# Kernel tuning notes

Measured on AMD Instinct MI355X. Metric: run time of the kernel, lower is better.

Reference implementation:

```python
import jax, jax.numpy as jnp
import numpy as np
import math

SEQ_LEN = 2048
D_MODEL = 512
HEADS = 8
HEAD_DIM = D_MODEL // HEADS
BATCH = 4


def setup_inputs() -> dict:
    key = jax.random.key(0)
    ks = jax.random.split(key, 12)
    s = 0.02
    return {
        "query": jax.random.normal(ks[0], (BATCH, SEQ_LEN, D_MODEL), dtype=jnp.float32),
        "Wq": jax.random.normal(ks[1], (D_MODEL, D_MODEL), dtype=jnp.float32) * s,
        "bq": jnp.zeros((D_MODEL,), dtype=jnp.float32),
        "Wk": jax.random.normal(ks[2], (D_MODEL, D_MODEL), dtype=jnp.float32) * s,
        "bk": jnp.zeros((D_MODEL,), dtype=jnp.float32),
        "Wv": jax.random.normal(ks[3], (D_MODEL, D_MODEL), dtype=jnp.float32) * s,
        "bv": jnp.zeros((D_MODEL,), dtype=jnp.float32),
        "Wp": jax.random.normal(ks[4], (D_MODEL, D_MODEL), dtype=jnp.float32) * s,
        "bp": jnp.zeros((D_MODEL,), dtype=jnp.float32),
        "logit_scale": jnp.full((HEADS, 1, 1), math.log(10.0), dtype=jnp.float32),
        "rpe": jax.random.normal(ks[5], (2 * SEQ_LEN - 1, HEADS), dtype=jnp.float32) * s,
    }


def reference(query, Wq, bq, Wk, bk, Wv, bv, Wp, bp, logit_scale, rpe):
    N, S, D = query.shape
    H = HEADS

    def split_heads(x):
        # reshape(N, S, head_dim, H) then permute(0, 3, 1, 2) -> (N, H, S, head_dim)
        return x.reshape(N, S, D // H, H).transpose(0, 3, 1, 2)

    q = split_heads(query @ Wq.T + bq)
    k = split_heads(query @ Wk.T + bk)  # key defaults to query
    v = split_heads(query @ Wv.T + bv)  # value defaults to key

    attn = jnp.einsum("bhqd,bhkd->bhqk", q, k) / math.sqrt(D)
    scale = jnp.exp(jnp.minimum(logit_scale, math.log(1.0 / 0.01)))  # (H,1,1)
    attn = attn * scale[None]

    # relative position bias: idx[i,j] = i - j + S - 1
    idx = jnp.arange(S)[:, None] - jnp.arange(S)[None, :] + (S - 1)  # (S,S)
    bias = jax.nn.sigmoid(rpe[idx].transpose(2, 0, 1))  # (H,S,S)
    attn = attn + bias[None]

    attn = jax.nn.softmax(attn, axis=-1)
    out = jnp.einsum("bhqk,bhkd->bhqd", attn, v)
    out = out.transpose(0, 2, 1, 3).reshape(N, S, D)
    return out @ Wp.T + bp
```

## Files before the change

### kernel.cpp

```cpp
#include <hip/hip_runtime.h>
#include <math.h>

#define N_B 4
#define SEQ 2048
#define DM  512
#define H_N 8
#define DH  64

typedef unsigned short ushort_t;
typedef __attribute__((ext_vector_type(8))) short short8_t;
typedef __attribute__((ext_vector_type(4))) float float4_t;

#define LOG2E 1.4426950408889634074f

__device__ __forceinline__ ushort_t f2bf(float f) {
    unsigned int x = __float_as_uint(f);
    unsigned int lsb = (x >> 16) & 1u;
    x += 0x7fffu + lsb;
    return (ushort_t)(x >> 16);
}
__device__ __forceinline__ unsigned int cvtpk_bf16(float a, float b) {
    unsigned int r;
    asm("v_cvt_pk_bf16_f32 %0, %1, %2" : "=v"(r) : "v"(a), "v"(b));
    return r;
}
__device__ __forceinline__ float fexp2(float x) {
#if __has_builtin(__builtin_amdgcn_exp2f)
    return __builtin_amdgcn_exp2f(x);
#else
    return exp2f(x);
#endif
}
__device__ __forceinline__ void gload_lds16(const ushort_t* g, ushort_t* l) {
    __builtin_amdgcn_global_load_lds((const __attribute__((address_space(1))) void*)g,
                                     (__attribute__((address_space(3))) void*)l,
                                     16, 0, 0);
}

#define Q4 1048576
#define W4 65536
#define RELN 4095
#define GTABN (H_N * RELN)
__global__ __launch_bounds__(256)
void prep(const float* __restrict__ query,
          const float* __restrict__ Wq, const float* __restrict__ Wk,
          const float* __restrict__ Wv, const float* __restrict__ Wp,
          const float* __restrict__ bq, const float* __restrict__ bk,
          const float* __restrict__ bv, const float* __restrict__ bp,
          const float* __restrict__ rpe,
          ushort_t* __restrict__ q16, ushort_t* __restrict__ w16,
          float* __restrict__ bcat, float* __restrict__ gtab)
{
    int i = blockIdx.x * 256 + threadIdx.x;
    if (i < Q4) {
        float4 x = ((const float4*)query)[i];
        uint2 p;
        p.x = cvtpk_bf16(x.x, x.y);
        p.y = cvtpk_bf16(x.z, x.w);
        ((uint2*)q16)[i] = p;
    } else if (i < Q4 + 4 * W4) {
        int wi = i - Q4;
        int w = wi >> 16;
        const float* W = (w == 0) ? Wq : (w == 1) ? Wk : (w == 2) ? Wv : Wp;
        float4 x = ((const float4*)W)[wi & (W4 - 1)];
        uint2 p;
        p.x = cvtpk_bf16(x.x, x.y);
        p.y = cvtpk_bf16(x.z, x.w);
        ((uint2*)w16)[wi] = p;
    } else if (i < Q4 + 4 * W4 + 512) {
        int bi = i - (Q4 + 4 * W4);
        int seg = bi >> 7;
        int off = bi & 127;
        const float* B = (seg == 0) ? bq : (seg == 1) ? bk : (seg == 2) ? bv : bp;
        ((float4*)bcat)[bi] = ((const float4*)B)[off];
    } else {
        int gi = i - (Q4 + 4 * W4 + 512);
        if (gi < GTABN) {
            int h = gi / RELN;
            int rel = gi - h * RELN;
            float4 v;
            #pragma unroll
            for (int c = 0; c < 4; c++) {
                int rr = rel - c;
                if (rr < 0) rr = 0;
                float x = rpe[rr * H_N + h];
                ((float*)&v)[c] = LOG2E / (1.0f + __expf(-x));
            }
            ((float4*)gtab)[gi] = v;
        }
    }
}

template<int MODE>
__global__ __launch_bounds__(256)
void mgemm(const ushort_t* __restrict__ A, const ushort_t* __restrict__ B,
           const float* __restrict__ bias,
           ushort_t* __restrict__ q_o, ushort_t* __restrict__ k_o,
           ushort_t* __restrict__ vt_o, float* __restrict__ p_o)
{
    __shared__ __align__(16) ushort_t As[128][64];
    __shared__ __align__(16) ushort_t Bs[128][64];

    const int t     = threadIdx.x;
    const int wid   = t >> 6;
    const int lane  = t & 63;
    const int lan16 = lane & 15;
    const int quad  = lane >> 4;
    const int wm    = (wid & 1) * 64;
    const int wn    = (wid >> 1) * 64;

    const int col0 = blockIdx.x * 128;
    const int row0 = blockIdx.y * 128;

    const int srow = lane >> 3;
    const int gchk = (lane & 7) ^ ((lane >> 3) & 7);
    const ushort_t* gA = A + (size_t)(row0 + wid * 8 + srow) * DM + gchk * 8;
    const ushort_t* gB = B + (size_t)(col0 + wid * 8 + srow) * DM + gchk * 8;

    float4_t acc[4][4];
    #pragma unroll
    for (int i = 0; i < 4; i++)
        #pragma unroll
        for (int j = 0; j < 4; j++) acc[i][j] = (float4_t){0.f, 0.f, 0.f, 0.f};

    const int sw = lan16 & 7;

    for (int k0 = 0; k0 < DM; k0 += 64) {
        __syncthreads();
        #pragma unroll
        for (int j = 0; j < 4; j++) {
            gload_lds16(gA + k0 + (size_t)j * 32 * DM, &As[j * 32 + wid * 8][0]);
            gload_lds16(gB + k0 + (size_t)j * 32 * DM, &Bs[j * 32 + wid * 8][0]);
        }
        asm volatile("s_waitcnt vmcnt(0)" ::: "memory");
        __syncthreads();

        #pragma unroll
        for (int kk = 0; kk < 2; kk++) {
            short8_t af[4], bf[4];
            #pragma unroll
            for (int i = 0; i < 4; i++) {
                af[i] = *(const short8_t*)&As[wm + i * 16 + lan16][((kk * 4 + quad) ^ sw) * 8];
                bf[i] = *(const short8_t*)&Bs[wn + i * 16 + lan16][((kk * 4 + quad) ^ sw) * 8];
            }
            #pragma unroll
            for (int i = 0; i < 4; i++)
                #pragma unroll
                for (int j = 0; j < 4; j++)
                    acc[i][j] = __builtin_amdgcn_mfma_f32_16x16x32_bf16(af[i], bf[j], acc[i][j], 0, 0, 0);
        }
    }

    #pragma unroll
    for (int j = 0; j < 4; j++) {
        int col = col0 + wn + j * 16 + lan16;
        float bv = bias[col];
        #pragma unroll
        for (int i = 0; i < 4; i++) {
            #pragma unroll
            for (int reg = 0; reg < 4; reg++) {
                int row = row0 + wm + i * 16 + quad * 4 + reg;
                float v = acc[i][j][reg] + bv;
                if (MODE == 0) {
                    int w = col >> 9;
                    int c = col & 511;
                    int hh = c & 7, dh = c >> 3;
                    int n = row >> 11, s = row & 2047;
                    if (w == 0)
                        q_o[(((size_t)(n * H_N + hh)) * SEQ + s) * DH + dh] = f2bf(v);
                    else if (w == 1)
                        k_o[(((size_t)(n * H_N + hh)) * SEQ + s) * DH + dh] = f2bf(v);
                    else
                        vt_o[(((size_t)(n * H_N + hh)) * DH + dh) * SEQ + s] = f2bf(v);
                } else {
                    p_o[(size_t)row * DM + col] = v;
                }
            }
        }
    }
}

__global__ __launch_bounds__(256)
void attn_k(const ushort_t* __restrict__ qw, const ushort_t* __restrict__ kw,
            const ushort_t* __restrict__ vt, const float* __restrict__ lsc,
            const float* __restrict__ gtab, ushort_t* __restrict__ ctx)
{
    __shared__ __align__(16) ushort_t K_s[2][64][72];
    __shared__ __align__(16) ushort_t VT_s[2][64][72];
    __shared__ __align__(16) unsigned int Pp[4][2][16][36];

    const int t     = threadIdx.x;
    const int wid   = t >> 6;
    const int lane  = t & 63;
    const int lan16 = lane & 15;
    const int quad  = lane >> 4;

    const int h  = blockIdx.x;
    const int qt = blockIdx.y;
    const int n  = blockIdx.z;
    const int q0 = qt * 128;

    const size_t headoff = ((size_t)(n * H_N + h)) * SEQ * DH;
    const ushort_t* qh  = qw + headoff;
    const ushort_t* kh  = kw + headoff;
    const ushort_t* vth = vt + headoff;

    float ls = lsc[h];
    const float lm = 4.60517018598809136804f;
    if (ls > lm) ls = lm;
    const float scale2 = __expf(ls) * 0.04419417382415921757f * LOG2E;

    const int qrow0 = q0 + wid * 32 + lan16;
    const float4* gt = (const float4*)gtab + (size_t)h * RELN + (qrow0 + 2047 - quad * 4);

    short8_t qb[2][2];
    #pragma unroll
    for (int qf = 0; qf < 2; qf++) {
        const ushort_t* src = qh + (size_t)(qrow0 + qf * 16) * DH + quad * 8;
        qb[qf][0] = *(const short8_t*)(src);
        qb[qf][1] = *(const short8_t*)(src + 32);
    }

    float l_run[2] = {0.f, 0.f};
    float4_t o[4][2];
    #pragma unroll
    for (int ds = 0; ds < 4; ds++)
        #pragma unroll
        for (int qf = 0; qf < 2; qf++) o[ds][qf] = (float4_t){0.f, 0.f, 0.f, 0.f};

    const int srow = t >> 2;
    const int sc   = (t & 3) * 16;
    const ushort_t* kbase = kh + (size_t)srow * DH + sc;
    const ushort_t* vbase = vth + (size_t)srow * SEQ + sc;

    uint4 kreg0 = *(const uint4*)(kbase);
    uint4 kreg1 = *(const uint4*)(kbase + 8);
    uint4 vreg0 = *(const uint4*)(vbase);
    uint4 vreg1 = *(const uint4*)(vbase + 8);
    float4 b4c[2][4];
    #pragma unroll
    for (int qf = 0; qf < 2; qf++)
        #pragma unroll
        for (int sub = 0; sub < 4; sub++) b4c[qf][sub] = gt[(qf - sub) * 16];
    *(uint4*)&K_s[0][srow][sc]      = kreg0;
    *(uint4*)&K_s[0][srow][sc + 8]  = kreg1;
    *(uint4*)&VT_s[0][srow][sc]     = vreg0;
    *(uint4*)&VT_s[0][srow][sc + 8] = vreg1;
    __syncthreads();
    int cur = 0;

    for (int j0 = 0; j0 < SEQ; j0 += 64) {
        const bool more = (j0 + 64 < SEQ);
        float4 b4n[2][4];
        if (more) {
            kreg0 = *(const uint4*)(kbase + (size_t)(j0 + 64) * DH);
            kreg1 = *(const uint4*)(kbase + (size_t)(j0 + 64) * DH + 8);
            vreg0 = *(const uint4*)(vbase + (j0 + 64));
            vreg1 = *(const uint4*)(vbase + (j0 + 64) + 8);
            const float4* gtp = gt - (j0 + 64);
            #pragma unroll
            for (int qf = 0; qf < 2; qf++)
                #pragma unroll
                for (int sub = 0; sub < 4; sub++) b4n[qf][sub] = gtp[(qf - sub) * 16];
        }

        float4_t st[4][2];
        #pragma unroll
        for (int sub = 0; sub < 4; sub++) {
            const ushort_t* kp = &K_s[cur][sub * 16 + lan16][quad * 8];
            short8_t ka0 = *(const short8_t*)(kp);
            short8_t ka1 = *(const short8_t*)(kp + 32);
            #pragma unroll
            for (int qf = 0; qf < 2; qf++) {
                float4_t a = (float4_t){0.f, 0.f, 0.f, 0.f};
                a = __builtin_amdgcn_mfma_f32_16x16x32_bf16(ka0, qb[qf][0], a, 0, 0, 0);
                a = __builtin_amdgcn_mfma_f32_16x16x32_bf16(ka1, qb[qf][1], a, 0, 0, 0);
                st[sub][qf] = a;
            }
        }

        #pragma unroll
        for (int qf = 0; qf < 2; qf++) {
            float ps = 0.f;
            #pragma unroll
            for (int sub = 0; sub < 4; sub++) {
                float e0 = fexp2(st[sub][qf][0] * scale2 + b4c[qf][sub].x);
                float e1 = fexp2(st[sub][qf][1] * scale2 + b4c[qf][sub].y);
                float e2 = fexp2(st[sub][qf][2] * scale2 + b4c[qf][sub].z);
                float e3 = fexp2(st[sub][qf][3] * scale2 + b4c[qf][sub].w);
                ps += (e0 + e1) + (e2 + e3);
                uint2 pw;
                pw.x = cvtpk_bf16(e0, e1);
                pw.y = cvtpk_bf16(e2, e3);
                *(uint2*)&Pp[wid][qf][lan16][sub * 8 + quad * 2] = pw;
            }
            l_run[qf] += ps;
        }
        asm volatile("s_waitcnt lgkmcnt(0)" ::: "memory");

        #pragma unroll
        for (int ks = 0; ks < 2; ks++) {
            short8_t pb[2];
            #pragma unroll
            for (int qf = 0; qf < 2; qf++)
                pb[qf] = *(const short8_t*)&Pp[wid][qf][lan16][ks * 16 + quad * 4];
            #pragma unroll
            for (int ds = 0; ds < 4; ds++) {
                short8_t va = *(const short8_t*)&VT_s[cur][ds * 16 + lan16][ks * 32 + quad * 8];
                #pragma unroll
                for (int qf = 0; qf < 2; qf++)
                    o[ds][qf] = __builtin_amdgcn_mfma_f32_16x16x32_bf16(va, pb[qf], o[ds][qf], 0, 0, 0);
            }
        }

        if (more) {
            *(uint4*)&K_s[cur ^ 1][srow][sc]      = kreg0;
            *(uint4*)&K_s[cur ^ 1][srow][sc + 8]  = kreg1;
            *(uint4*)&VT_s[cur ^ 1][srow][sc]     = vreg0;
            *(uint4*)&VT_s[cur ^ 1][srow][sc + 8] = vreg1;
            __syncthreads();
            cur ^= 1;
            #pragma unroll
            for (int qf = 0; qf < 2; qf++)
                #pragma unroll
                for (int sub = 0; sub < 4; sub++) b4c[qf][sub] = b4n[qf][sub];
        }
    }

    #pragma unroll
    for (int qf = 0; qf < 2; qf++) {
        float l = l_run[qf];
        l += __shfl_xor(l, 16);
        l += __shfl_xor(l, 32);
        float inv = 1.0f / l;
        int row = qrow0 + qf * 16;
        size_t base = ((size_t)n * SEQ + row) * DM + h * DH;
        #pragma unroll
        for (int ds = 0; ds < 4; ds++) {
            uint2 p;
            p.x = cvtpk_bf16(o[ds][qf][0] * inv, o[ds][qf][1] * inv);
            p.y = cvtpk_bf16(o[ds][qf][2] * inv, o[ds][qf][3] * inv);
            *(uint2*)(ctx + base + ds * 16 + quad * 4) = p;
        }
    }
}

extern "C" void kernel_launch(void* const* d_in, const int* in_sizes, int n_in,
                              void* d_out, int out_size, void* d_ws, size_t ws_size,
                              hipStream_t stream) {
    const float* query = (const float*)d_in[0];
    const float* Wq  = (const float*)d_in[1];
    const float* bq  = (const float*)d_in[2];
    const float* Wk  = (const float*)d_in[3];
    const float* bk  = (const float*)d_in[4];
    const float* Wv  = (const float*)d_in[5];
    const float* bv  = (const float*)d_in[6];
    const float* Wp  = (const float*)d_in[7];
    const float* bp  = (const float*)d_in[8];
    const float* lsc = (const float*)d_in[9];
    const float* rpe = (const float*)d_in[10];

    const size_t QEL = (size_t)N_B * SEQ * DM;
    const size_t WEL = (size_t)DM * DM;
    char* ws = (char*)d_ws;
    ushort_t* q16  = (ushort_t*)(ws);
    ushort_t* w16  = q16 + QEL;
    float*    bcat = (float*)(w16 + 4 * WEL);
    float*    gtab = bcat + 2048;
    ushort_t* qb   = (ushort_t*)(gtab + 4 * GTABN);
    ushort_t* kb   = qb + QEL;
    ushort_t* vtb  = kb + QEL;
    ushort_t* ctx  = vtb + QEL;

    const int PREPN = Q4 + 4 * W4 + 512 + GTABN;
    prep<<<(PREPN + 255) / 256, 256, 0, stream>>>(
        query, Wq, Wk, Wv, Wp, bq, bk, bv, bp, rpe, q16, w16, bcat, gtab);

    dim3 g1(1536 / 128, (N_B * SEQ) / 128);
    mgemm<0><<<g1, 256, 0, stream>>>(q16, w16, bcat, qb, kb, vtb, nullptr);

    dim3 ga(H_N, SEQ / 128, N_B);
    attn_k<<<ga, 256, 0, stream>>>(qb, kb, vtb, lsc, gtab, ctx);

    dim3 g2(DM / 128, (N_B * SEQ) / 128);
    mgemm<1><<<g2, 256, 0, stream>>>(ctx, w16 + 3 * WEL, bcat + 1536,
                                     nullptr, nullptr, nullptr, (float*)d_out);
}
```

Measured before the change: 205.9 us.

## Permute QKV weight rows per head and stage epilogue through LDS for vector stores

The prep kernel now reorders the Q/K/V weight rows and biases so that each 128-column GEMM tile covers two contiguous heads in head-dim order. The QKV GEMM epilogue writes bf16 results into an LDS tile that reuses the A/B buffers, transposing it for V. It then issues coalesced 16-byte stores to the head-split q/k/vT buffers instead of scattered 2-byte stores. This trades extra LDS traffic and a barrier for much better global write coalescing.

```diff
diff --git a/kernel.cpp b/kernel.cpp
--- a/kernel.cpp
+++ b/kernel.cpp
@@ -62,19 +62,24 @@
         int wi = i - Q4;
         int w = wi >> 16;
         const float* W = (w == 0) ? Wq : (w == 1) ? Wk : (w == 2) ? Wv : Wp;
-        float4 x = ((const float4*)W)[wi & (W4 - 1)];
+        int gwi = wi & (W4 - 1);
+        int c = gwi >> 7;
+        int g = gwi & 127;
+        float4 x = ((const float4*)W)[gwi];
         uint2 p;
         p.x = cvtpk_bf16(x.x, x.y);
         p.y = cvtpk_bf16(x.z, x.w);
-        ((uint2*)w16)[wi] = p;
-    } else if (i < Q4 + 4 * W4 + 512) {
+        int c2 = (w < 3) ? (((c & 7) << 6) | (c >> 3)) : c;
+        ((uint2*)w16)[w * W4 + c2 * 128 + g] = p;
+    } else if (i < Q4 + 4 * W4 + 2048) {
         int bi = i - (Q4 + 4 * W4);
-        int seg = bi >> 7;
-        int off = bi & 127;
+        int seg = bi >> 9;
+        int c = bi & 511;
         const float* B = (seg == 0) ? bq : (seg == 1) ? bk : (seg == 2) ? bv : bp;
-        ((float4*)bcat)[bi] = ((const float4*)B)[off];
+        int c2 = (seg < 3) ? (((c & 7) << 6) | (c >> 3)) : c;
+        bcat[seg * 512 + c2] = B[c];
     } else {
-        int gi = i - (Q4 + 4 * W4 + 512);
+        int gi = i - (Q4 + 4 * W4 + 2048);
         if (gi < GTABN) {
             int h = gi / RELN;
             int rel = gi - h * RELN;
@@ -98,8 +103,12 @@
            ushort_t* __restrict__ q_o, ushort_t* __restrict__ k_o,
            ushort_t* __restrict__ vt_o, float* __restrict__ p_o)
 {
-    __shared__ __align__(16) ushort_t As[128][64];
-    __shared__ __align__(16) ushort_t Bs[128][64];
+    __shared__ __align__(16) union SM {
+        struct { ushort_t A[128][64]; ushort_t B[128][64]; } ab;
+        ushort_t C[128][128];
+    } sm;
+    ushort_t (&As)[128][64] = sm.ab.A;
+    ushort_t (&Bs)[128][64] = sm.ab.B;
 
     const int t     = threadIdx.x;
     const int wid   = t >> 6;
@@ -151,31 +160,78 @@
         }
     }
 
-    #pragma unroll
-    for (int j = 0; j < 4; j++) {
-        int col = col0 + wn + j * 16 + lan16;
-        float bv = bias[col];
-        #pragma unroll
-        for (int i = 0; i < 4; i++) {
-            #pragma unroll
-            for (int reg = 0; reg < 4; reg++) {
-                int row = row0 + wm + i * 16 + quad * 4 + reg;
-                float v = acc[i][j][reg] + bv;
-                if (MODE == 0) {
-                    int w = col >> 9;
-                    int c = col & 511;
-                    int hh = c & 7, dh = c >> 3;
-                    int n = row >> 11, s = row & 2047;
-                    if (w == 0)
-                        q_o[(((size_t)(n * H_N + hh)) * SEQ + s) * DH + dh] = f2bf(v);
-                    else if (w == 1)
-                        k_o[(((size_t)(n * H_N + hh)) * SEQ + s) * DH + dh] = f2bf(v);
-                    else
-                        vt_o[(((size_t)(n * H_N + hh)) * DH + dh) * SEQ + s] = f2bf(v);
-                } else {
-                    p_o[(size_t)row * DM + col] = v;
+    if (MODE == 1) {
+        #pragma unroll
+        for (int j = 0; j < 4; j++) {
+            int col = col0 + wn + j * 16 + lan16;
+            float bv = bias[col];
+            #pragma unroll
+            for (int i = 0; i < 4; i++) {
+                #pragma unroll
+                for (int reg = 0; reg < 4; reg++) {
+                    int row = row0 + wm + i * 16 + quad * 4 + reg;
+                    p_o[(size_t)row * DM + col] = acc[i][j][reg] + bv;
                 }
             }
+        }
+        return;
+    }
+
+    const int w = col0 >> 9;
+    __syncthreads();
+
+    if (w < 2) {
+        #pragma unroll
+        for (int j = 0; j < 4; j++) {
+            float bv = bias[col0 + wn + j * 16 + lan16];
+            #pragma unroll
+            for (int i = 0; i < 4; i++)
+                #pragma unroll
+                for (int reg = 0; reg < 4; reg++)
+                    sm.C[wm + i * 16 + quad * 4 + reg][wn + j * 16 + lan16] =
+                        f2bf(acc[i][j][reg] + bv);
+        }
+    } else {
+        #pragma unroll
+        for (int j = 0; j < 4; j++) {
+            float bv = bias[col0 + wn + j * 16 + lan16];
+            #pragma unroll
+            for (int i = 0; i < 4; i++) {
+                uint2 pw;
+                pw.x = cvtpk_bf16(acc[i][j][0] + bv, acc[i][j][1] + bv);
+                pw.y = cvtpk_bf16(acc[i][j][2] + bv, acc[i][j][3] + bv);
+                *(uint2*)&sm.C[wn + j * 16 + lan16][wm + i * 16 + quad * 4] = pw;
+            }
+        }
+    }
+    __syncthreads();
+
+    const int n   = row0 >> 11;
+    const int s0  = row0 & 2047;
+    const int hh0 = (col0 & 511) >> 6;
+
+    if (w < 2) {
+        ushort_t* dst = (w == 0) ? q_o : k_o;
+        #pragma unroll
+        for (int it = 0; it < 8; it++) {
+            int ch  = it * 256 + t;
+            int s   = ch >> 4;
+            int c16 = ch & 15;
+            int head = hh0 + (c16 >> 3);
+            int dq   = (c16 & 7) * 8;
+            size_t a = (((size_t)(n * H_N + head)) * SEQ + (s0 + s)) * DH + dq;
+            *(uint4*)(dst + a) = *(const uint4*)&sm.C[s][c16 * 8];
+        }
+    } else {
+        #pragma unroll
+        for (int it = 0; it < 8; it++) {
+            int ch = it * 256 + t;
+            int r  = ch >> 4;
+            int sg = ch & 15;
+            int head = hh0 + (r >> 6);
+            int dh   = r & 63;
+            size_t a = (((size_t)(n * H_N + head)) * DH + dh) * SEQ + s0 + sg * 8;
+            *(uint4*)(vt_o + a) = *(const uint4*)&sm.C[r][sg * 8];
         }
     }
 }
@@ -372,7 +428,7 @@
     ushort_t* vtb  = kb + QEL;
     ushort_t* ctx  = vtb + QEL;
 
-    const int PREPN = Q4 + 4 * W4 + 512 + GTABN;
+    const int PREPN = Q4 + 4 * W4 + 2048 + GTABN;
     prep<<<(PREPN + 255) / 256, 256, 0, stream>>>(
         query, Wq, Wk, Wv, Wp, bq, bk, bv, bp, rpe, q16, w16, bcat, gtab);
 
```

Result: faster. 188.1 us (-8.6%).
